# Kernel optimization log

Measured on AMD Instinct MI355X. Metric: run time of the kernel, lower is better.

The kernel has to match this reference:

```python
import jax, jax.numpy as jnp
import numpy as np

N_NODES = 50000
N_EDGES = 800000
N_GRAPHS = 500
BN_EPS = 1e-5
DIMS = [128, 256, 256, 256, 256, 256, 256]  # in, conv1..5, concat


def setup_inputs() -> dict:
    key = jax.random.key(0)
    ks = jax.random.split(key, 16)
    inp = {
        "x": jax.random.normal(ks[0], (N_NODES, DIMS[0]), jnp.float32),
        "edge_index": jax.random.randint(ks[1], (2, N_EDGES), 0, N_NODES, dtype=jnp.int64),
        "batch": jnp.sort(jax.random.randint(ks[2], (N_NODES,), 0, N_GRAPHS, dtype=jnp.int64)),
    }
    for i in range(6):
        fin, fout = DIMS[i], DIMS[i + 1]
        inp[f"W{i+1}"] = jax.random.normal(ks[3 + i], (fin, fout), jnp.float32) / np.sqrt(fin)
        inp[f"b{i+1}"] = jnp.zeros((fout,), jnp.float32)
    for i in range(5):
        inp[f"gamma{i+1}"] = jnp.ones((DIMS[i + 1],), jnp.float32)
        inp[f"beta{i+1}"] = jnp.zeros((DIMS[i + 1],), jnp.float32)
    return inp


def _gcn_conv(x, src, dst, dinv, W, b):
    # PyG GCNConv: add self-loops, symmetric norm D^-1/2 (A+I) D^-1/2, x@W then aggregate, + bias
    xw = x @ W  # [N, Fout]
    norm = dinv[src] * dinv[dst]  # [E]
    agg = jax.ops.segment_sum(norm[:, None] * xw[src], dst, num_segments=N_NODES)
    agg = agg + (dinv * dinv)[:, None] * xw  # self-loop contribution
    return agg + b


def _bn(x, gamma, beta):
    # BatchNorm1d, training-mode batch statistics (biased variance, as torch)
    m = x.mean(axis=0)
    v = x.var(axis=0)
    return gamma * (x - m) * jax.lax.rsqrt(v + BN_EPS) + beta


def reference(x, edge_index, batch,
              W1, b1, W2, b2, W3, b3, W4, b4, W5, b5, W6, b6,
              gamma1, beta1, gamma2, beta2, gamma3, beta3, gamma4, beta4, gamma5, beta5):
    src, dst = edge_index[0], edge_index[1]
    # degree of A + I (counted over destination nodes)
    deg = jnp.zeros((N_NODES,), x.dtype).at[dst].add(1.0) + 1.0
    dinv = jax.lax.rsqrt(deg)
    h = x
    convs = [(W1, b1), (W2, b2), (W3, b3), (W4, b4), (W5, b5)]
    bns = [(gamma1, beta1), (gamma2, beta2), (gamma3, beta3), (gamma4, beta4), (gamma5, beta5)]
    for (W, b), (g, be) in zip(convs, bns):
        h = jax.nn.relu(_gcn_conv(h, src, dst, dinv, W, b))
        h = _bn(h, g, be)
    h = jax.nn.relu(_gcn_conv(h, src, dst, dinv, W6, b6))
    # global_add_pool; dropout is identity in eval mode
    return jax.ops.segment_sum(h, batch, num_segments=N_GRAPHS)
```

## Files before the change

kernel.cpp:

```cpp
#include <hip/hip_runtime.h>

#define N_NODES 50000
#define N_EDGES 800000
#define N_GRAPHS 500
#define BN_EPS 1e-5f
#define F 256
#define SCAN_BLOCKS ((N_NODES + 255) / 256)
#define NPART 64

typedef short short8 __attribute__((ext_vector_type(8)));
typedef short short4v __attribute__((ext_vector_type(4)));
typedef float f32x4 __attribute__((ext_vector_type(4)));
typedef _Float16 h16x8 __attribute__((ext_vector_type(8)));

__global__ void k_hist(const int* __restrict__ dst, int* __restrict__ cnt) {
    int e = blockIdx.x * blockDim.x + threadIdx.x;
    if (e < N_EDGES) atomicAdd(&cnt[dst[e]], 1);
}

__global__ void k_dinv(const int* __restrict__ cnt, float* __restrict__ dinv,
                       float* __restrict__ normsum) {
    int n = blockIdx.x * blockDim.x + threadIdx.x;
    if (n < N_NODES) {
        float d = rsqrtf((float)cnt[n] + 1.0f);
        dinv[n] = d;
        normsum[n] = d * d;
    }
}

__global__ void k_scan1(const int* __restrict__ cnt, int* __restrict__ rowptr,
                        int* __restrict__ bsum) {
    __shared__ int s[256];
    int tid = threadIdx.x;
    int i = blockIdx.x * 256 + tid;
    int v = (i < N_NODES) ? cnt[i] : 0;
    s[tid] = v;
    __syncthreads();
    for (int off = 1; off < 256; off <<= 1) {
        int add = (tid >= off) ? s[tid - off] : 0;
        __syncthreads();
        s[tid] += add;
        __syncthreads();
    }
    if (i < N_NODES) rowptr[i] = s[tid] - v;
    if (tid == 255) bsum[blockIdx.x] = s[255];
}

__global__ void k_scan2(int* __restrict__ bsum) {
    __shared__ int s[256];
    int tid = threadIdx.x;
    int v = (tid < SCAN_BLOCKS) ? bsum[tid] : 0;
    s[tid] = v;
    __syncthreads();
    for (int off = 1; off < 256; off <<= 1) {
        int add = (tid >= off) ? s[tid - off] : 0;
        __syncthreads();
        s[tid] += add;
        __syncthreads();
    }
    if (tid < SCAN_BLOCKS) bsum[tid] = s[tid] - v;
}

__global__ void k_scan3(int* __restrict__ rowptr, const int* __restrict__ bsum) {
    int i = blockIdx.x * 256 + threadIdx.x;
    if (i < N_NODES) rowptr[i] += bsum[blockIdx.x];
    if (i == 0) rowptr[N_NODES] = N_EDGES;
}

__global__ void k_scatter(const int* __restrict__ src, const int* __restrict__ dst,
                          const float* __restrict__ dinv, const int* __restrict__ rowptr,
                          int* __restrict__ fill, int2* __restrict__ epair,
                          float* __restrict__ normsum) {
    int e = blockIdx.x * 256 + threadIdx.x;
    if (e >= N_EDGES) return;
    int s = src[e], d = dst[e];
    float norm = dinv[s] * dinv[d];
    int slot = rowptr[d] + atomicAdd(&fill[d], 1);
    epair[slot] = make_int2(s, __float_as_int(norm));
    atomicAdd(&normsum[d], norm);
}

__global__ void k_pack(const float* __restrict__ W, short* __restrict__ hi,
                       short* __restrict__ lo, int K) {
    int idx = blockIdx.x * 256 + threadIdx.x;
    if (idx >= 256 * K) return;
    int n = idx / K, k = idx - n * K;
    float f = W[(size_t)k * 256 + n];
    unsigned u = __builtin_bit_cast(unsigned, f);
    hi[idx] = (short)(u >> 16);
    float hf = __builtin_bit_cast(float, u & 0xFFFF0000u);
    lo[idx] = (short)(__builtin_bit_cast(unsigned, f - hf) >> 16);
}

__global__ __launch_bounds__(256)
void k_wfold(const float* __restrict__ W, const float* __restrict__ mulk,
             const float* __restrict__ addk, short* __restrict__ hi,
             short* __restrict__ lo, float* __restrict__ rowvec) {
    __shared__ float red[256];
    const int n = blockIdx.x;
    const int k = threadIdx.x;
    float w = W[(size_t)k * 256 + n];
    float f = w * mulk[k];
    unsigned u = __builtin_bit_cast(unsigned, f);
    hi[(size_t)n * 256 + k] = (short)(u >> 16);
    float hf = __builtin_bit_cast(float, u & 0xFFFF0000u);
    lo[(size_t)n * 256 + k] = (short)(__builtin_bit_cast(unsigned, f - hf) >> 16);
    red[k] = addk[k] * w;
    __syncthreads();
    for (int off = 128; off > 0; off >>= 1) {
        if (k < off) red[k] += red[k + off];
        __syncthreads();
    }
    if (k == 0) rowvec[n] = red[0];
}

__global__ void k_splitx(const float* __restrict__ x, short* __restrict__ hi,
                         short* __restrict__ lo) {
    int idx = blockIdx.x * 256 + threadIdx.x;
    if (idx >= N_NODES * 32) return;
    float4 v = reinterpret_cast<const float4*>(x)[idx];
    float vv[4] = {v.x, v.y, v.z, v.w};
    short4v h4, l4;
    #pragma unroll
    for (int j = 0; j < 4; ++j) {
        unsigned u = __builtin_bit_cast(unsigned, vv[j]);
        h4[j] = (short)(u >> 16);
        float hf = __builtin_bit_cast(float, u & 0xFFFF0000u);
        l4[j] = (short)(__builtin_bit_cast(unsigned, vv[j] - hf) >> 16);
    }
    *reinterpret_cast<short4v*>(&hi[(size_t)idx * 4]) = h4;
    *reinterpret_cast<short4v*>(&lo[(size_t)idx * 4]) = l4;
}

#define BK 32
__global__ __launch_bounds__(256)
void k_gemm_mfma(const short* __restrict__ Ahi, const short* __restrict__ Alo,
                 const short* __restrict__ Bhi, const short* __restrict__ Blo,
                 _Float16* __restrict__ C, int M, int K) {
    __shared__ unsigned As[2][128 * 16];
    const int tid  = threadIdx.x;
    const int lane = tid & 63;
    const int w    = tid >> 6;
    const int wr   = (w >> 1) * 64;
    const int wc   = (w & 1) * 64;
    const int bid  = blockIdx.x;
    const int bx   = (bid >> 4) * 8 + (bid & 7);
    const int by   = (bid >> 3) & 1;
    const int brow = bx * 128;
    const int bcol = by * 128;

    f32x4 acc[4][4];
    #pragma unroll
    for (int m = 0; m < 4; ++m)
        #pragma unroll
        for (int n = 0; n < 4; ++n) acc[m][n] = (f32x4){0.f, 0.f, 0.f, 0.f};

    const int lr = tid >> 1;
    const int lk = (tid & 1) * 16;
    const int grow = brow + lr;
    const bool rowok = grow < M;
    const short* Ahp = Ahi + (size_t)grow * K + lk;
    const short* Alp = Alo + (size_t)grow * K + lk;
    const int NS = K / BK;

    uint4 ph0, ph1, pl0, pl1;
    auto load_pf = [&](int s) {
        if (rowok) {
            ph0 = *reinterpret_cast<const uint4*>(Ahp + s * BK);
            ph1 = *reinterpret_cast<const uint4*>(Ahp + s * BK + 8);
            pl0 = *reinterpret_cast<const uint4*>(Alp + s * BK);
            pl1 = *reinterpret_cast<const uint4*>(Alp + s * BK + 8);
        } else {
            ph0 = ph1 = pl0 = pl1 = make_uint4(0, 0, 0, 0);
        }
    };

    load_pf(0);

    const int sw = (lr >> 1) & 3;
    const int c0 = (tid & 1) * 2;
    unsigned* dh0 = &As[0][lr * 16 + ((c0 ^ sw) << 2)];
    unsigned* dh1 = &As[0][lr * 16 + (((c0 + 1) ^ sw) << 2)];
    unsigned* dl0 = &As[1][lr * 16 + ((c0 ^ sw) << 2)];
    unsigned* dl1 = &As[1][lr * 16 + (((c0 + 1) ^ sw) << 2)];

    for (int s = 0; s < NS; ++s) {
        __syncthreads();
        *reinterpret_cast<uint4*>(dh0) = ph0;
        *reinterpret_cast<uint4*>(dh1) = ph1;
        *reinterpret_cast<uint4*>(dl0) = pl0;
        *reinterpret_cast<uint4*>(dl1) = pl1;
        if (s + 1 < NS) load_pf(s + 1);
        __syncthreads();

        short8 bh[4], bl[4];
        const int kb = s * BK + (lane >> 4) * 8;
        #pragma unroll
        for (int n = 0; n < 4; ++n) {
            int col = bcol + wc + n * 16 + (lane & 15);
            bh[n] = *reinterpret_cast<const short8*>(Bhi + (size_t)col * K + kb);
            bl[n] = *reinterpret_cast<const short8*>(Blo + (size_t)col * K + kb);
        }
        #pragma unroll
        for (int m = 0; m < 4; ++m) {
            int row = wr + m * 16 + (lane & 15);
            int c = lane >> 4;
            int sw2 = (row >> 1) & 3;
            const unsigned* ph = &As[0][row * 16 + ((c ^ sw2) << 2)];
            const unsigned* pl = &As[1][row * 16 + ((c ^ sw2) << 2)];
            short8 ah = *reinterpret_cast<const short8*>(ph);
            short8 al = *reinterpret_cast<const short8*>(pl);
            #pragma unroll
            for (int n = 0; n < 4; ++n) {
                acc[m][n] = __builtin_amdgcn_mfma_f32_16x16x32_bf16(ah, bh[n], acc[m][n], 0, 0, 0);
                acc[m][n] = __builtin_amdgcn_mfma_f32_16x16x32_bf16(al, bh[n], acc[m][n], 0, 0, 0);
                acc[m][n] = __builtin_amdgcn_mfma_f32_16x16x32_bf16(ah, bl[n], acc[m][n], 0, 0, 0);
            }
        }
    }

    #pragma unroll
    for (int m = 0; m < 4; ++m) {
        #pragma unroll
        for (int n = 0; n < 4; ++n) {
            int col = bcol + wc + n * 16 + (lane & 15);
            #pragma unroll
            for (int j = 0; j < 4; ++j) {
                int row = brow + wr + m * 16 + (lane >> 4) * 4 + j;
                if (row < M) C[(size_t)row * 256 + col] = (_Float16)acc[m][n][j];
            }
        }
    }
}

#define BATCH 8
template<int MODE>
__global__ __launch_bounds__(256)
void k_agg2(const _Float16* __restrict__ xw, const float* __restrict__ dinv,
            const float* __restrict__ normsum, const int* __restrict__ rowptr,
            const int2* __restrict__ epair, const float* __restrict__ bias,
            const float* __restrict__ rowvec, short* __restrict__ hhi,
            short* __restrict__ hlo, float* __restrict__ hf32,
            float* __restrict__ stats) {
    __shared__ float red[2][4][256];
    const int lane = threadIdx.x & 63;
    const int wave = threadIdx.x >> 6;
    const int half = lane >> 5;
    const int fl   = lane & 31;
    const int n    = blockIdx.x * 4 + wave;

    const h16x8* xw8 = reinterpret_cast<const h16x8*>(xw);

    float acc[8];
    if (half == 0) {
        float d = dinv[n];
        float sl = d * d;
        h16x8 sv = xw8[(size_t)n * 32 + fl];
        #pragma unroll
        for (int j = 0; j < 8; ++j) acc[j] = sl * (float)sv[j];
    } else {
        #pragma unroll
        for (int j = 0; j < 8; ++j) acc[j] = 0.f;
    }

    const int beg = rowptr[n], end = rowptr[n + 1];
    int i = beg + half;

    if (i < end) {
        int ecur[BATCH]; float wcur[BATCH];
        #pragma unroll
        for (int k = 0; k < BATCH; ++k) {
            int idx = i + 2 * k;
            bool ok = idx < end;
            int2 p = epair[ok ? idx : (end - 1)];
            ecur[k] = p.x;
            wcur[k] = ok ? __int_as_float(p.y) : 0.f;
        }
        while (true) {
            h16x8 r[BATCH];
            #pragma unroll
            for (int k = 0; k < BATCH; ++k)
                r[k] = xw8[(size_t)ecur[k] * 32 + fl];

            int inext = i + 2 * BATCH;
            bool more = inext < end;
            int enxt[BATCH]; float wnxt[BATCH];
            if (more) {
                #pragma unroll
                for (int k = 0; k < BATCH; ++k) {
                    int idx = inext + 2 * k;
                    bool ok = idx < end;
                    int2 p = epair[ok ? idx : (end - 1)];
                    enxt[k] = p.x;
                    wnxt[k] = ok ? __int_as_float(p.y) : 0.f;
                }
            }
            #pragma unroll
            for (int k = 0; k < BATCH; ++k)
                #pragma unroll
                for (int j = 0; j < 8; ++j)
                    acc[j] = fmaf(wcur[k], (float)r[k][j], acc[j]);
            if (!more) break;
            i = inext;
            #pragma unroll
            for (int k = 0; k < BATCH; ++k) { ecur[k] = enxt[k]; wcur[k] = wnxt[k]; }
        }
    }

    #pragma unroll
    for (int j = 0; j < 8; ++j) acc[j] += __shfl_xor(acc[j], 32, 64);

    if (half == 0) {
        float4 b0 = *reinterpret_cast<const float4*>(&bias[fl * 8]);
        float4 b1 = *reinterpret_cast<const float4*>(&bias[fl * 8 + 4]);
        float4 r0 = *reinterpret_cast<const float4*>(&rowvec[fl * 8]);
        float4 r1 = *reinterpret_cast<const float4*>(&rowvec[fl * 8 + 4]);
        float bv[8] = {b0.x, b0.y, b0.z, b0.w, b1.x, b1.y, b1.z, b1.w};
        float rv[8] = {r0.x, r0.y, r0.z, r0.w, r1.x, r1.y, r1.z, r1.w};
        float S = normsum[n];
        #pragma unroll
        for (int j = 0; j < 8; ++j)
            acc[j] = fmaxf(acc[j] + fmaf(S, rv[j], bv[j]), 0.f);

        if (MODE == 0) {
            unsigned hw[4], lw[4];
            #pragma unroll
            for (int p = 0; p < 4; ++p) {
                float f0 = acc[2 * p], f1 = acc[2 * p + 1];
                unsigned u0 = __builtin_bit_cast(unsigned, f0);
                unsigned u1 = __builtin_bit_cast(unsigned, f1);
                hw[p] = (u1 & 0xFFFF0000u) | (u0 >> 16);
                float h0 = __builtin_bit_cast(float, u0 & 0xFFFF0000u);
                float h1 = __builtin_bit_cast(float, u1 & 0xFFFF0000u);
                lw[p] = (__builtin_bit_cast(unsigned, f1 - h1) & 0xFFFF0000u) |
                        (__builtin_bit_cast(unsigned, f0 - h0) >> 16);
            }
            *reinterpret_cast<uint4*>(&hhi[(size_t)n * 256 + fl * 8]) =
                make_uint4(hw[0], hw[1], hw[2], hw[3]);
            *reinterpret_cast<uint4*>(&hlo[(size_t)n * 256 + fl * 8]) =
                make_uint4(lw[0], lw[1], lw[2], lw[3]);
            float4 o0 = make_float4(acc[0], acc[1], acc[2], acc[3]);
            float4 o1 = make_float4(acc[4], acc[5], acc[6], acc[7]);
            float4 q0 = make_float4(acc[0]*acc[0], acc[1]*acc[1], acc[2]*acc[2], acc[3]*acc[3]);
            float4 q1 = make_float4(acc[4]*acc[4], acc[5]*acc[5], acc[6]*acc[6], acc[7]*acc[7]);
            *reinterpret_cast<float4*>(&red[0][wave][fl * 8])     = o0;
            *reinterpret_cast<float4*>(&red[0][wave][fl * 8 + 4]) = o1;
            *reinterpret_cast<float4*>(&red[1][wave][fl * 8])     = q0;
            *reinterpret_cast<float4*>(&red[1][wave][fl * 8 + 4]) = q1;
        } else {
            *reinterpret_cast<float4*>(&hf32[(size_t)n * 256 + fl * 8]) =
                make_float4(acc[0], acc[1], acc[2], acc[3]);
            *reinterpret_cast<float4*>(&hf32[(size_t)n * 256 + fl * 8 + 4]) =
                make_float4(acc[4], acc[5], acc[6], acc[7]);
        }
    }

    if (MODE == 0) {
        __syncthreads();
        int t = threadIdx.x;
        float s = red[0][0][t] + red[0][1][t] + red[0][2][t] + red[0][3][t];
        float q = red[1][0][t] + red[1][1][t] + red[1][2][t] + red[1][3][t];
        float* part = stats + (size_t)(blockIdx.x & (NPART - 1)) * 512;
        atomicAdd(&part[t], s);
        atomicAdd(&part[256 + t], q);
    }
}

__global__ void k_bnfinalize(const float* __restrict__ stats,
                             const float* __restrict__ gamma, const float* __restrict__ beta,
                             float* __restrict__ mulk, float* __restrict__ addk) {
    int f = threadIdx.x;
    float s = 0.f, q = 0.f;
    for (int p = 0; p < NPART; ++p) {
        s += stats[(size_t)p * 512 + f];
        q += stats[(size_t)p * 512 + 256 + f];
    }
    float m = s * (1.0f / N_NODES);
    float var = q * (1.0f / N_NODES) - m * m;
    float sc = gamma[f] * rsqrtf(var + BN_EPS);
    mulk[f] = sc;
    addk[f] = beta[f] - m * sc;
}

template<int ROWS>
__global__ __launch_bounds__(256)
void k_pool(const float* __restrict__ h, const int* __restrict__ batch,
            float* __restrict__ out) {
    const int f = threadIdx.x;
    const int r0 = blockIdx.x * ROWS;
    float acc = 0.f;
    int cur = -1;
    for (int i = 0; i < ROWS; ++i) {
        int n = r0 + i;
        if (n >= N_NODES) break;
        int g = batch[n];
        float v = h[(size_t)n * F + f];
        if (g != cur) {
            if (cur >= 0) atomicAdd(&out[(size_t)cur * F + f], acc);
            cur = g; acc = v;
        } else {
            acc += v;
        }
    }
    if (cur >= 0) atomicAdd(&out[(size_t)cur * F + f], acc);
}

extern "C" void kernel_launch(void* const* d_in, const int* in_sizes, int n_in,
                              void* d_out, int out_size, void* d_ws, size_t ws_size,
                              hipStream_t stream) {
    const float* x     = (const float*)d_in[0];
    const int*   ei    = (const int*)d_in[1];
    const int*   batch = (const int*)d_in[2];
    const float* W[6], *bias[6], *gamma[5], *beta[5];
    for (int i = 0; i < 6; ++i) {
        W[i]    = (const float*)d_in[3 + 2 * i];
        bias[i] = (const float*)d_in[4 + 2 * i];
    }
    for (int i = 0; i < 5; ++i) {
        gamma[i] = (const float*)d_in[15 + 2 * i];
        beta[i]  = (const float*)d_in[16 + 2 * i];
    }
    float* out = (float*)d_out;

    char* ws = (char*)d_ws;
    size_t off = 0;
    auto alloc = [&](size_t bytes) {
        void* p = ws + off;
        off = (off + bytes + 255) & ~(size_t)255;
        return p;
    };
    int*   cnt      = (int*)  alloc(N_NODES * 4);
    int*   rowptr   = (int*)  alloc((N_NODES + 1) * 4);
    int*   bsum     = (int*)  alloc(256 * 4);
    float* dinv     = (float*)alloc(N_NODES * 4);
    float* normsum  = (float*)alloc(N_NODES * 4);
    int2*  epair    = (int2*) alloc((size_t)N_EDGES * 8);
    float* mulk     = (float*)alloc(F * 4);
    float* addk     = (float*)alloc(F * 4);
    float* rowvec   = (float*)alloc(F * 4);
    float* statsAll = (float*)alloc((size_t)5 * NPART * 512 * 4);
    short* Whi[6]; short* Wlo[6];
    for (int l = 0; l < 6; ++l) {
        int K = (l == 0) ? 128 : 256;
        Whi[l] = (short*)alloc((size_t)256 * K * 2);
        Wlo[l] = (short*)alloc((size_t)256 * K * 2);
    }
    short* xhi = (short*)alloc((size_t)N_NODES * 128 * 2);
    short* xlo = (short*)alloc((size_t)N_NODES * 128 * 2);
    short* hhi = (short*)alloc((size_t)N_NODES * F * 2);
    short* hlo = (short*)alloc((size_t)N_NODES * F * 2);
    _Float16* xw   = (_Float16*)alloc((size_t)N_NODES * F * 2);
    float*    hfin = (float*)   alloc((size_t)N_NODES * F * 4);

    const int* src = ei;
    const int* dst = ei + N_EDGES;

    hipMemsetAsync(cnt, 0, N_NODES * 4, stream);
    hipMemsetAsync(out, 0, (size_t)N_GRAPHS * F * 4, stream);
    hipMemsetAsync(rowvec, 0, F * 4, stream);
    hipMemsetAsync(statsAll, 0, (size_t)5 * NPART * 512 * 4, stream);
    k_hist<<<(N_EDGES + 255) / 256, 256, 0, stream>>>(dst, cnt);
    k_dinv<<<(N_NODES + 255) / 256, 256, 0, stream>>>(cnt, dinv, normsum);
    k_scan1<<<SCAN_BLOCKS, 256, 0, stream>>>(cnt, rowptr, bsum);
    k_scan2<<<1, 256, 0, stream>>>(bsum);
    k_scan3<<<SCAN_BLOCKS, 256, 0, stream>>>(rowptr, bsum);
    hipMemsetAsync(cnt, 0, N_NODES * 4, stream);
    k_scatter<<<(N_EDGES + 255) / 256, 256, 0, stream>>>(src, dst, dinv, rowptr, cnt,
                                                         epair, normsum);
    k_pack<<<(256 * 128 + 255) / 256, 256, 0, stream>>>(W[0], Whi[0], Wlo[0], 128);
    k_splitx<<<(N_NODES * 32 + 255) / 256, 256, 0, stream>>>(x, xhi, xlo);

    const int aggGrid = N_NODES / 4;
    for (int l = 0; l < 6; ++l) {
        const int K = (l == 0) ? 128 : 256;
        const short* Ah = (l == 0) ? xhi : hhi;
        const short* Al = (l == 0) ? xlo : hlo;
        k_gemm_mfma<<<784, 256, 0, stream>>>(Ah, Al, Whi[l], Wlo[l], xw, N_NODES, K);

        if (l < 5) {
            float* stats = statsAll + (size_t)l * NPART * 512;
            k_agg2<0><<<aggGrid, 256, 0, stream>>>(xw, dinv, normsum, rowptr, epair,
                                                   bias[l], rowvec, hhi, hlo, nullptr, stats);
            k_bnfinalize<<<1, F, 0, stream>>>(stats, gamma[l], beta[l], mulk, addk);
            k_wfold<<<256, 256, 0, stream>>>(W[l + 1], mulk, addk,
                                             Whi[l + 1], Wlo[l + 1], rowvec);
        } else {
            k_agg2<1><<<aggGrid, 256, 0, stream>>>(xw, dinv, normsum, rowptr, epair,
                                                   bias[l], rowvec, nullptr, nullptr,
                                                   hfin, nullptr);
            k_pool<128><<<(N_NODES + 127) / 128, 256, 0, stream>>>(hfin, batch, out);
        }
    }
}
```

Before: 1.145 ms.

## Double-buffer GEMM LDS tile, fuse BN finalize into wfold, vectorize edge preprocessing

The GEMM now keeps two LDS buffers and writes the next tile after the MFMA loop, which removes one barrier per k-step. The BN finalize kernel is merged into k_wfold, so each of the 256 blocks recomputes the column statistics and one launch is saved. The per-node normsum is now summed inside the aggregation kernel, which removes an atomic per edge in scatter. Histogram and scatter read four edges per thread, and a device copy of rowptr replaces the memset plus add. The cost is redundant stats reduction in every wfold block, plus edges written into their CSR slots in nondeterministic order.

```diff
diff --git a/kernel.cpp b/kernel.cpp
--- a/kernel.cpp
+++ b/kernel.cpp
@@ -14,18 +14,18 @@
 typedef _Float16 h16x8 __attribute__((ext_vector_type(8)));
 
 __global__ void k_hist(const int* __restrict__ dst, int* __restrict__ cnt) {
-    int e = blockIdx.x * blockDim.x + threadIdx.x;
-    if (e < N_EDGES) atomicAdd(&cnt[dst[e]], 1);
-}
-
-__global__ void k_dinv(const int* __restrict__ cnt, float* __restrict__ dinv,
-                       float* __restrict__ normsum) {
+    int e0 = (blockIdx.x * blockDim.x + threadIdx.x) * 4;
+    if (e0 >= N_EDGES) return;
+    int4 d4 = *reinterpret_cast<const int4*>(&dst[e0]);
+    atomicAdd(&cnt[d4.x], 1);
+    atomicAdd(&cnt[d4.y], 1);
+    atomicAdd(&cnt[d4.z], 1);
+    atomicAdd(&cnt[d4.w], 1);
+}
+
+__global__ void k_dinv(const int* __restrict__ cnt, float* __restrict__ dinv) {
     int n = blockIdx.x * blockDim.x + threadIdx.x;
-    if (n < N_NODES) {
-        float d = rsqrtf((float)cnt[n] + 1.0f);
-        dinv[n] = d;
-        normsum[n] = d * d;
-    }
+    if (n < N_NODES) dinv[n] = rsqrtf((float)cnt[n] + 1.0f);
 }
 
 __global__ void k_scan1(const int* __restrict__ cnt, int* __restrict__ rowptr,
@@ -68,16 +68,20 @@
 }
 
 __global__ void k_scatter(const int* __restrict__ src, const int* __restrict__ dst,
-                          const float* __restrict__ dinv, const int* __restrict__ rowptr,
-                          int* __restrict__ fill, int2* __restrict__ epair,
-                          float* __restrict__ normsum) {
-    int e = blockIdx.x * 256 + threadIdx.x;
-    if (e >= N_EDGES) return;
-    int s = src[e], d = dst[e];
-    float norm = dinv[s] * dinv[d];
-    int slot = rowptr[d] + atomicAdd(&fill[d], 1);
-    epair[slot] = make_int2(s, __float_as_int(norm));
-    atomicAdd(&normsum[d], norm);
+                          const float* __restrict__ dinv, int* __restrict__ fillptr,
+                          int2* __restrict__ epair) {
+    int e0 = (blockIdx.x * blockDim.x + threadIdx.x) * 4;
+    if (e0 >= N_EDGES) return;
+    int4 s4 = *reinterpret_cast<const int4*>(&src[e0]);
+    int4 d4 = *reinterpret_cast<const int4*>(&dst[e0]);
+    int ss[4] = {s4.x, s4.y, s4.z, s4.w};
+    int dd[4] = {d4.x, d4.y, d4.z, d4.w};
+    #pragma unroll
+    for (int j = 0; j < 4; ++j) {
+        float norm = dinv[ss[j]] * dinv[dd[j]];
+        int slot = atomicAdd(&fillptr[dd[j]], 1);
+        epair[slot] = make_int2(ss[j], __float_as_int(norm));
+    }
 }
 
 __global__ void k_pack(const float* __restrict__ W, short* __restrict__ hi,
@@ -93,19 +97,29 @@
 }
 
 __global__ __launch_bounds__(256)
-void k_wfold(const float* __restrict__ W, const float* __restrict__ mulk,
-             const float* __restrict__ addk, short* __restrict__ hi,
-             short* __restrict__ lo, float* __restrict__ rowvec) {
+void k_wfold(const float* __restrict__ W, const float* __restrict__ stats,
+             const float* __restrict__ gamma, const float* __restrict__ beta,
+             short* __restrict__ hi, short* __restrict__ lo,
+             float* __restrict__ rowvec) {
     __shared__ float red[256];
     const int n = blockIdx.x;
     const int k = threadIdx.x;
+    float s = 0.f, q = 0.f;
+    for (int p = 0; p < NPART; ++p) {
+        s += stats[(size_t)p * 512 + k];
+        q += stats[(size_t)p * 512 + 256 + k];
+    }
+    float m = s * (1.0f / N_NODES);
+    float var = q * (1.0f / N_NODES) - m * m;
+    float mulk = gamma[k] * rsqrtf(var + BN_EPS);
+    float addk = beta[k] - m * mulk;
     float w = W[(size_t)k * 256 + n];
-    float f = w * mulk[k];
+    float f = w * mulk;
     unsigned u = __builtin_bit_cast(unsigned, f);
     hi[(size_t)n * 256 + k] = (short)(u >> 16);
     float hf = __builtin_bit_cast(float, u & 0xFFFF0000u);
     lo[(size_t)n * 256 + k] = (short)(__builtin_bit_cast(unsigned, f - hf) >> 16);
-    red[k] = addk[k] * w;
+    red[k] = addk * w;
     __syncthreads();
     for (int off = 128; off > 0; off >>= 1) {
         if (k < off) red[k] += red[k + off];
@@ -137,7 +151,7 @@
 void k_gemm_mfma(const short* __restrict__ Ahi, const short* __restrict__ Alo,
                  const short* __restrict__ Bhi, const short* __restrict__ Blo,
                  _Float16* __restrict__ C, int M, int K) {
-    __shared__ unsigned As[2][128 * 16];
+    __shared__ unsigned As[2][2][128 * 16];
     const int tid  = threadIdx.x;
     const int lane = tid & 63;
     const int w    = tid >> 6;
@@ -175,21 +189,19 @@
         }
     };
 
+    const int sw  = (lr >> 1) & 3;
+    const int c0  = (tid & 1) * 2;
+    const int off0 = lr * 16 + ((c0 ^ sw) << 2);
+    const int off1 = lr * 16 + (((c0 + 1) ^ sw) << 2);
+
     load_pf(0);
-
-    const int sw = (lr >> 1) & 3;
-    const int c0 = (tid & 1) * 2;
-    unsigned* dh0 = &As[0][lr * 16 + ((c0 ^ sw) << 2)];
-    unsigned* dh1 = &As[0][lr * 16 + (((c0 + 1) ^ sw) << 2)];
-    unsigned* dl0 = &As[1][lr * 16 + ((c0 ^ sw) << 2)];
-    unsigned* dl1 = &As[1][lr * 16 + (((c0 + 1) ^ sw) << 2)];
+    *reinterpret_cast<uint4*>(&As[0][0][off0]) = ph0;
+    *reinterpret_cast<uint4*>(&As[0][0][off1]) = ph1;
+    *reinterpret_cast<uint4*>(&As[0][1][off0]) = pl0;
+    *reinterpret_cast<uint4*>(&As[0][1][off1]) = pl1;
 
     for (int s = 0; s < NS; ++s) {
-        __syncthreads();
-        *reinterpret_cast<uint4*>(dh0) = ph0;
-        *reinterpret_cast<uint4*>(dh1) = ph1;
-        *reinterpret_cast<uint4*>(dl0) = pl0;
-        *reinterpret_cast<uint4*>(dl1) = pl1;
+        const int cur = s & 1;
         if (s + 1 < NS) load_pf(s + 1);
         __syncthreads();
 
@@ -206,8 +218,8 @@
             int row = wr + m * 16 + (lane & 15);
             int c = lane >> 4;
             int sw2 = (row >> 1) & 3;
-            const unsigned* ph = &As[0][row * 16 + ((c ^ sw2) << 2)];
-            const unsigned* pl = &As[1][row * 16 + ((c ^ sw2) << 2)];
+            const unsigned* ph = &As[cur][0][row * 16 + ((c ^ sw2) << 2)];
+            const unsigned* pl = &As[cur][1][row * 16 + ((c ^ sw2) << 2)];
             short8 ah = *reinterpret_cast<const short8*>(ph);
             short8 al = *reinterpret_cast<const short8*>(pl);
             #pragma unroll
@@ -217,6 +229,12 @@
                 acc[m][n] = __builtin_amdgcn_mfma_f32_16x16x32_bf16(ah, bl[n], acc[m][n], 0, 0, 0);
             }
         }
+        if (s + 1 < NS) {
+            *reinterpret_cast<uint4*>(&As[cur ^ 1][0][off0]) = ph0;
+            *reinterpret_cast<uint4*>(&As[cur ^ 1][0][off1]) = ph1;
+            *reinterpret_cast<uint4*>(&As[cur ^ 1][1][off0]) = pl0;
+            *reinterpret_cast<uint4*>(&As[cur ^ 1][1][off1]) = pl1;
+        }
     }
 
     #pragma unroll
@@ -237,11 +255,10 @@
 template<int MODE>
 __global__ __launch_bounds__(256)
 void k_agg2(const _Float16* __restrict__ xw, const float* __restrict__ dinv,
-            const float* __restrict__ normsum, const int* __restrict__ rowptr,
-            const int2* __restrict__ epair, const float* __restrict__ bias,
-            const float* __restrict__ rowvec, short* __restrict__ hhi,
-            short* __restrict__ hlo, float* __restrict__ hf32,
-            float* __restrict__ stats) {
+            const int* __restrict__ rowptr, const int2* __restrict__ epair,
+            const float* __restrict__ bias, const float* __restrict__ rowvec,
+            short* __restrict__ hhi, short* __restrict__ hlo,
+            float* __restrict__ hf32, float* __restrict__ stats) {
     __shared__ float red[2][4][256];
     const int lane = threadIdx.x & 63;
     const int wave = threadIdx.x >> 6;
@@ -252,15 +269,18 @@
     const h16x8* xw8 = reinterpret_cast<const h16x8*>(xw);
 
     float acc[8];
+    float wsum;
     if (half == 0) {
         float d = dinv[n];
         float sl = d * d;
         h16x8 sv = xw8[(size_t)n * 32 + fl];
         #pragma unroll
         for (int j = 0; j < 8; ++j) acc[j] = sl * (float)sv[j];
+        wsum = sl;
     } else {
         #pragma unroll
         for (int j = 0; j < 8; ++j) acc[j] = 0.f;
+        wsum = 0.f;
     }
 
     const int beg = rowptr[n], end = rowptr[n + 1];
@@ -296,10 +316,12 @@
                 }
             }
             #pragma unroll
-            for (int k = 0; k < BATCH; ++k)
+            for (int k = 0; k < BATCH; ++k) {
+                wsum += wcur[k];
                 #pragma unroll
                 for (int j = 0; j < 8; ++j)
                     acc[j] = fmaf(wcur[k], (float)r[k][j], acc[j]);
+            }
             if (!more) break;
             i = inext;
             #pragma unroll
@@ -309,6 +331,7 @@
 
     #pragma unroll
     for (int j = 0; j < 8; ++j) acc[j] += __shfl_xor(acc[j], 32, 64);
+    wsum += __shfl_xor(wsum, 32, 64);
 
     if (half == 0) {
         float4 b0 = *reinterpret_cast<const float4*>(&bias[fl * 8]);
@@ -317,10 +340,9 @@
         float4 r1 = *reinterpret_cast<const float4*>(&rowvec[fl * 8 + 4]);
         float bv[8] = {b0.x, b0.y, b0.z, b0.w, b1.x, b1.y, b1.z, b1.w};
         float rv[8] = {r0.x, r0.y, r0.z, r0.w, r1.x, r1.y, r1.z, r1.w};
-        float S = normsum[n];
         #pragma unroll
         for (int j = 0; j < 8; ++j)
-            acc[j] = fmaxf(acc[j] + fmaf(S, rv[j], bv[j]), 0.f);
+            acc[j] = fmaxf(acc[j] + fmaf(wsum, rv[j], bv[j]), 0.f);
 
         if (MODE == 0) {
             unsigned hw[4], lw[4];
@@ -366,22 +388,6 @@
     }
 }
 
-__global__ void k_bnfinalize(const float* __restrict__ stats,
-                             const float* __restrict__ gamma, const float* __restrict__ beta,
-                             float* __restrict__ mulk, float* __restrict__ addk) {
-    int f = threadIdx.x;
-    float s = 0.f, q = 0.f;
-    for (int p = 0; p < NPART; ++p) {
-        s += stats[(size_t)p * 512 + f];
-        q += stats[(size_t)p * 512 + 256 + f];
-    }
-    float m = s * (1.0f / N_NODES);
-    float var = q * (1.0f / N_NODES) - m * m;
-    float sc = gamma[f] * rsqrtf(var + BN_EPS);
-    mulk[f] = sc;
-    addk[f] = beta[f] - m * sc;
-}
-
 template<int ROWS>
 __global__ __launch_bounds__(256)
 void k_pool(const float* __restrict__ h, const int* __restrict__ batch,
@@ -431,12 +437,10 @@
     };
     int*   cnt      = (int*)  alloc(N_NODES * 4);
     int*   rowptr   = (int*)  alloc((N_NODES + 1) * 4);
+    int*   fillptr  = (int*)  alloc(N_NODES * 4);
     int*   bsum     = (int*)  alloc(256 * 4);
     float* dinv     = (float*)alloc(N_NODES * 4);
-    float* normsum  = (float*)alloc(N_NODES * 4);
     int2*  epair    = (int2*) alloc((size_t)N_EDGES * 8);
-    float* mulk     = (float*)alloc(F * 4);
-    float* addk     = (float*)alloc(F * 4);
     float* rowvec   = (float*)alloc(F * 4);
     float* statsAll = (float*)alloc((size_t)5 * NPART * 512 * 4);
     short* Whi[6]; short* Wlo[6];
@@ -459,14 +463,13 @@
     hipMemsetAsync(out, 0, (size_t)N_GRAPHS * F * 4, stream);
     hipMemsetAsync(rowvec, 0, F * 4, stream);
     hipMemsetAsync(statsAll, 0, (size_t)5 * NPART * 512 * 4, stream);
-    k_hist<<<(N_EDGES + 255) / 256, 256, 0, stream>>>(dst, cnt);
-    k_dinv<<<(N_NODES + 255) / 256, 256, 0, stream>>>(cnt, dinv, normsum);
+    k_hist<<<(N_EDGES / 4 + 255) / 256, 256, 0, stream>>>(dst, cnt);
+    k_dinv<<<(N_NODES + 255) / 256, 256, 0, stream>>>(cnt, dinv);
     k_scan1<<<SCAN_BLOCKS, 256, 0, stream>>>(cnt, rowptr, bsum);
     k_scan2<<<1, 256, 0, stream>>>(bsum);
     k_scan3<<<SCAN_BLOCKS, 256, 0, stream>>>(rowptr, bsum);
-    hipMemsetAsync(cnt, 0, N_NODES * 4, stream);
-    k_scatter<<<(N_EDGES + 255) / 256, 256, 0, stream>>>(src, dst, dinv, rowptr, cnt,
-                                                         epair, normsum);
+    hipMemcpyAsync(fillptr, rowptr, N_NODES * 4, hipMemcpyDeviceToDevice, stream);
+    k_scatter<<<(N_EDGES / 4 + 255) / 256, 256, 0, stream>>>(src, dst, dinv, fillptr, epair);
     k_pack<<<(256 * 128 + 255) / 256, 256, 0, stream>>>(W[0], Whi[0], Wlo[0], 128);
     k_splitx<<<(N_NODES * 32 + 255) / 256, 256, 0, stream>>>(x, xhi, xlo);
 
@@ -479,13 +482,13 @@
 
         if (l < 5) {
             float* stats = statsAll + (size_t)l * NPART * 512;
-            k_agg2<0><<<aggGrid, 256, 0, stream>>>(xw, dinv, normsum, rowptr, epair,
-                                                   bias[l], rowvec, hhi, hlo, nullptr, stats);
-            k_bnfinalize<<<1, F, 0, stream>>>(stats, gamma[l], beta[l], mulk, addk);
-            k_wfold<<<256, 256, 0, stream>>>(W[l + 1], mulk, addk,
+            k_agg2<0><<<aggGrid, 256, 0, stream>>>(xw, dinv, rowptr, epair,
+                                                   bias[l], rowvec, hhi, hlo,
+                                                   nullptr, stats);
+            k_wfold<<<256, 256, 0, stream>>>(W[l + 1], stats, gamma[l], beta[l],
                                              Whi[l + 1], Wlo[l + 1], rowvec);
         } else {
-            k_agg2<1><<<aggGrid, 256, 0, stream>>>(xw, dinv, normsum, rowptr, epair,
+            k_agg2<1><<<aggGrid, 256, 0, stream>>>(xw, dinv, rowptr, epair,
                                                    bias[l], rowvec, nullptr, nullptr,
                                                    hfin, nullptr);
             k_pool<128><<<(N_NODES + 127) / 128, 256, 0, stream>>>(hfin, batch, out);
```

Result: faster. 1.076 ms (-6.0%).
